# Kernel tuning notes

Measured on AMD Instinct MI355X. Metric: run time of the kernel, lower is better.

## Reference

```python
import jax, jax.numpy as jnp
import numpy as np

B, E, H, F, L, A = 256, 1024, 1024, 2048, 196, 512
C_RATIO, H_RATIO = 0.5, 0.5


def setup_inputs() -> dict:
    key = jax.random.key(0)
    ks = jax.random.split(key, 20)
    u = lambda k, shape: jax.random.uniform(k, shape, jnp.float32, -0.1, 0.1)
    return {
        "xt": jax.random.normal(ks[0], (B, E), jnp.float32),
        "att_seq": jax.random.normal(ks[1], (B, L, F), jnp.float32),
        "h": jax.random.normal(ks[2], (B, H), jnp.float32),
        "c": jax.random.normal(ks[3], (B, H), jnp.float32),
        "Wi": u(ks[4], (4 * H, E)), "bi": u(ks[5], (4 * H,)),
        "Wh": u(ks[6], (4 * H, H)), "bh": u(ks[7], (4 * H,)),
        "Wz": u(ks[8], (4 * H, F)), "bz": u(ks[9], (4 * H,)),
        "Wa": u(ks[10], (A, F)), "ba": u(ks[11], (A,)),
        "Wha": u(ks[12], (A, H)), "bha": u(ks[13], (A,)),
        "Wo": u(ks[14], (1, A)), "bo": u(ks[15], (1,)),
    }


def reference(xt, att_seq, h, c, Wi, bi, Wh, bh, Wz, bz, Wa, ba, Wha, bha, Wo, bo):
    # attention scoring: tanh(att_2_att_h(att) + h_2_att_h(h)) -> scalar per location
    att_linear = jnp.einsum("blf,af->bla", att_seq, Wa) + ba          # [B,L,A]
    h_linear = h @ Wha.T + bha                                        # [B,A]
    att_h = jnp.tanh(att_linear + h_linear[:, None, :])               # [B,L,A]
    scores = jnp.einsum("bla,a->bl", att_h, Wo[0]) + bo[0]            # [B,L]
    w = jax.nn.softmax(scores, axis=-1)                               # [B,L]
    z = jnp.einsum("bl,blf->bf", w, att_seq)                          # [B,F] context

    # fused LSTM gates
    sums = (xt @ Wi.T + bi) + (h @ Wh.T + bh) + (z @ Wz.T + bz)       # [B,4H]
    i_g = jax.nn.sigmoid(sums[:, 0 * H:1 * H])
    f_g = jax.nn.sigmoid(sums[:, 1 * H:2 * H])
    o_g = jax.nn.sigmoid(sums[:, 2 * H:3 * H])
    g = jnp.tanh(sums[:, 3 * H:4 * H])

    # zoneout blending (training mode; dropout prob is 0 -> identity)
    next_c = c * C_RATIO + (1.0 - C_RATIO) * (f_g * c + i_g * g)
    next_h = h * H_RATIO + (1.0 - H_RATIO) * (o_g * jnp.tanh(next_c))
    return next_h, next_h, next_c  # (output, state_h, state_c)
```

## Files before the change

### kernel.cpp

```cpp
#include <hip/hip_runtime.h>

#define B_ 256
#define E_ 1024
#define H_ 1024
#define F_ 2048
#define L_ 196
#define A_ 512
#define ML (B_ * L_)

typedef __attribute__((ext_vector_type(8))) short short8;
typedef __attribute__((ext_vector_type(4))) float f32x4;

__device__ __forceinline__ unsigned short f2bf(float x) {
  unsigned u = __float_as_uint(x);
  unsigned r = (u + 0x7FFFu + ((u >> 16) & 1u)) >> 16;
  return (unsigned short)r;
}
__device__ __forceinline__ float bf2f(unsigned short u) {
  return __uint_as_float((unsigned)u << 16);
}
__device__ __forceinline__ float fast_tanh(float x) {
  x = fminf(fmaxf(x, -15.f), 15.f);
  float e = __expf(2.f * x);
  return (e - 1.f) / (e + 1.f);
}
__device__ __forceinline__ float sigmoidf_(float x) {
  return 1.f / (1.f + __expf(-x));
}

#define GLOAD_LDS(gptr, lptr) \
  __builtin_amdgcn_global_load_lds( \
      (const __attribute__((address_space(1))) void*)(gptr), \
      (__attribute__((address_space(3))) void*)(lptr), 16, 0, 0)

#define SBAR() asm volatile("s_barrier" ::: "memory")

__global__ void cast_wx_k(const float* __restrict__ Wa, const float* __restrict__ Wha,
                          const float* __restrict__ Wi, const float* __restrict__ Wh,
                          const float* __restrict__ Wz, const float* __restrict__ xt,
                          const float* __restrict__ h,
                          unsigned short* __restrict__ WaB, unsigned short* __restrict__ WhaB,
                          unsigned short* __restrict__ WgB, unsigned short* __restrict__ AgB) {
  size_t i = ((size_t)blockIdx.x * 256 + threadIdx.x) * 8;
  const float* src;
  unsigned short* dst;
  if (i < 1048576) { src = Wa + i; dst = WaB + i; }
  else if (i < 1572864) { src = Wha + (i - 1048576); dst = WhaB + (i - 1048576); }
  else if (i < 18350080) {
    size_t off = i - 1572864;
    int row = (int)(off >> 12), col = (int)(off & 4095);
    if (col < 1024)       src = Wi + (size_t)row * 1024 + col;
    else if (col < 2048)  src = Wh + (size_t)row * 1024 + (col - 1024);
    else                  src = Wz + (size_t)row * 2048 + (col - 2048);
    dst = WgB + off;
  } else {
    size_t off = i - 18350080;
    int row = (int)(off >> 11), col = (int)(off & 2047);
    src = (col < 1024) ? (xt + (size_t)row * 1024 + col) : (h + (size_t)row * 1024 + (col - 1024));
    dst = AgB + (size_t)row * 4096 + col;
  }
  float4 a = *reinterpret_cast<const float4*>(src);
  float4 b = *reinterpret_cast<const float4*>(src + 4);
  short8 o;
  o[0] = (short)f2bf(a.x); o[1] = (short)f2bf(a.y); o[2] = (short)f2bf(a.z); o[3] = (short)f2bf(a.w);
  o[4] = (short)f2bf(b.x); o[5] = (short)f2bf(b.y); o[6] = (short)f2bf(b.z); o[7] = (short)f2bf(b.w);
  *reinterpret_cast<short8*>(dst) = o;
}

__global__ __launch_bounds__(256, 2)
void hlin_gemm_k(const unsigned short* __restrict__ AgB, const unsigned short* __restrict__ WhaB,
                 const float* __restrict__ bha, float* __restrict__ hlin) {
  __shared__ unsigned short As[2][64 * 64];
  __shared__ unsigned short Bs[2][128 * 64];
  const int tid = threadIdx.x;
  const int lane = tid & 63, wid = tid >> 6;
  const int wm = wid >> 1, wn = wid & 1;
  const int m0 = blockIdx.y * 64;
  const int n0 = blockIdx.x * 128;
  const int g16 = lane >> 4, l16 = lane & 15;
  const int l7 = l16 & 7;
  f32x4 acc[2][4] = {};

#define STAGE_HL(BUF, KK)                                                                      \
  {                                                                                            \
    _Pragma("unroll")                                                                          \
    for (int it = 0; it < 2; ++it) {                                                           \
      int idx = it * 256 + tid;                                                                \
      int row = idx >> 3;                                                                      \
      int kc = (idx & 7) ^ (row & 7);                                                          \
      GLOAD_LDS(AgB + (size_t)(m0 + row) * 4096 + 1024 + (KK) + kc * 8, &As[BUF][idx * 8]);    \
    }                                                                                          \
    _Pragma("unroll")                                                                          \
    for (int it = 0; it < 4; ++it) {                                                           \
      int idx = it * 256 + tid;                                                                \
      int row = idx >> 3;                                                                      \
      int kc = (idx & 7) ^ (row & 7);                                                          \
      GLOAD_LDS(WhaB + (size_t)(n0 + row) * 1024 + (KK) + kc * 8, &Bs[BUF][idx * 8]);          \
    }                                                                                          \
  }

  STAGE_HL(0, 0);
  STAGE_HL(1, 64);
  asm volatile("s_waitcnt vmcnt(6)" ::: "memory");
  SBAR();
  int cur = 0;
  for (int k0 = 0; k0 < 1024; k0 += 64) {
    #pragma unroll
    for (int ks = 0; ks < 2; ++ks) {
      const int ko = ((ks * 4 + g16) ^ l7) << 3;
      short8 af[2], bfr[4];
      #pragma unroll
      for (int mi = 0; mi < 2; ++mi)
        af[mi] = *reinterpret_cast<const short8*>(&As[cur][(wm * 32 + mi * 16 + l16) * 64 + ko]);
      #pragma unroll
      for (int ni = 0; ni < 4; ++ni)
        bfr[ni] = *reinterpret_cast<const short8*>(&Bs[cur][(wn * 64 + ni * 16 + l16) * 64 + ko]);
      #pragma unroll
      for (int mi = 0; mi < 2; ++mi)
        #pragma unroll
        for (int ni = 0; ni < 4; ++ni)
          acc[mi][ni] = __builtin_amdgcn_mfma_f32_16x16x32_bf16(af[mi], bfr[ni], acc[mi][ni], 0, 0, 0);
    }
    SBAR();
    if (k0 + 128 < 1024) {
      STAGE_HL(cur, k0 + 128);
      asm volatile("s_waitcnt vmcnt(6)" ::: "memory");
    } else {
      asm volatile("s_waitcnt vmcnt(0)" ::: "memory");
    }
    SBAR();
    cur ^= 1;
  }
#undef STAGE_HL

  #pragma unroll
  for (int ni = 0; ni < 4; ++ni) {
    int col = n0 + wn * 64 + ni * 16 + l16;
    float bv = bha[col];
    #pragma unroll
    for (int mi = 0; mi < 2; ++mi)
      #pragma unroll
      for (int j = 0; j < 4; ++j) {
        int m = m0 + wm * 32 + mi * 16 + g16 * 4 + j;
        hlin[(size_t)m * A_ + col] = acc[mi][ni][j] + bv;
      }
  }
}

template <bool WB>
__global__ __launch_bounds__(256, 2)
void score_fuse_k(const float* __restrict__ att, unsigned short* __restrict__ attB,
                  const unsigned short* __restrict__ WaB,
                  const float* __restrict__ hlin, const float* __restrict__ ba,
                  const float* __restrict__ Wo, float* __restrict__ scores8) {
  __shared__ unsigned short As[2][128 * 64];
  __shared__ unsigned short Bs[2][128 * 64];
  const int tid = threadIdx.x;
  const int lane = tid & 63, wid = tid >> 6;
  const int wm = wid >> 1, wn = wid & 1;
  const int logical = (blockIdx.x & 7) * 196 + (blockIdx.x >> 3);
  const int m0 = (logical >> 2) * 128;
  const int n0 = (logical & 3) * 128;
  const int g16 = lane >> 4, l16 = lane & 15;
  const int l7 = l16 & 7;
  f32x4 acc[4][4] = {};
  float4 a_reg[8];

#define LOADA(KK)                                                                        \
  {                                                                                      \
    _Pragma("unroll")                                                                    \
    for (int it = 0; it < 8; ++it) {                                                     \
      int idx = it * 256 + tid;                                                          \
      int row = idx >> 4, kf = idx & 15;                                                 \
      a_reg[it] = *reinterpret_cast<const float4*>(att + (size_t)(m0 + row) * F_ + (KK) + kf * 4); \
    }                                                                                    \
  }
#define GLDB(BUF, KK)                                                                    \
  {                                                                                      \
    _Pragma("unroll")                                                                    \
    for (int it = 0; it < 4; ++it) {                                                     \
      int idx = it * 256 + tid;                                                          \
      int row = idx >> 3;                                                                \
      int kc = (idx & 7) ^ (row & 7);                                                    \
      GLOAD_LDS(WaB + (size_t)(n0 + row) * F_ + (KK) + kc * 8, &Bs[BUF][idx * 8]);       \
    }                                                                                    \
  }
#define WRITEA(BUF, KK)                                                                  \
  {                                                                                      \
    _Pragma("unroll")                                                                    \
    for (int it = 0; it < 8; ++it) {                                                     \
      int idx = it * 256 + tid;                                                          \
      int row = idx >> 4, kf = idx & 15;                                                 \
      float4 v = a_reg[it];                                                              \
      ushort4 o;                                                                         \
      o.x = f2bf(v.x); o.y = f2bf(v.y); o.z = f2bf(v.z); o.w = f2bf(v.w);                \
      int el = row * 64 + (((kf >> 1) ^ (row & 7)) << 3) + ((kf & 1) << 2);              \
      *reinterpret_cast<ushort4*>(&As[BUF][el]) = o;                                     \
      if (WB && n0 == 0)                                                                 \
        *reinterpret_cast<ushort4*>(attB + (size_t)(m0 + row) * F_ + (KK) + kf * 4) = o; \
    }                                                                                    \
  }

  LOADA(0);
  GLDB(0, 0);
  asm volatile("s_waitcnt vmcnt(0)" ::: "memory");
  WRITEA(0, 0);
  LOADA(64);
  GLDB(1, 64);
  asm volatile("s_waitcnt lgkmcnt(0)" ::: "memory");
  SBAR();

  int cur = 0;
  for (int k0 = 0; k0 < F_; k0 += 64) {
    #pragma unroll
    for (int ks = 0; ks < 2; ++ks) {
      const int ko = ((ks * 4 + g16) ^ l7) << 3;
      short8 af[4], bfr[4];
      #pragma unroll
      for (int mi = 0; mi < 4; ++mi)
        af[mi] = *reinterpret_cast<const short8*>(&As[cur][(wm * 64 + mi * 16 + l16) * 64 + ko]);
      #pragma unroll
      for (int ni = 0; ni < 4; ++ni)
        bfr[ni] = *reinterpret_cast<const short8*>(&Bs[cur][(wn * 64 + ni * 16 + l16) * 64 + ko]);
      #pragma unroll
      for (int mi = 0; mi < 4; ++mi)
        #pragma unroll
        for (int ni = 0; ni < 4; ++ni)
          acc[mi][ni] = __builtin_amdgcn_mfma_f32_16x16x32_bf16(af[mi], bfr[ni], acc[mi][ni], 0, 0, 0);
    }
    SBAR();
    if (k0 + 64 < F_) {
      asm volatile("s_waitcnt vmcnt(0)" ::: "memory");
      WRITEA(cur ^ 1, k0 + 64);
      if (k0 + 128 < F_) {
        LOADA(k0 + 128);
        GLDB(cur, k0 + 128);
      }
      asm volatile("s_waitcnt lgkmcnt(0)" ::: "memory");
    }
    SBAR();
    cur ^= 1;
  }
#undef LOADA
#undef GLDB
#undef WRITEA

  float wo_v[4], ba_v[4];
  int a_v[4];
  #pragma unroll
  for (int ni = 0; ni < 4; ++ni) {
    int a = n0 + wn * 64 + ni * 16 + l16;
    a_v[ni] = a; wo_v[ni] = Wo[a]; ba_v[ni] = ba[a];
  }
  const int slot = (n0 >> 7) * 2 + wn;
  #pragma unroll
  for (int mi = 0; mi < 4; ++mi) {
    float rs[4];
    #pragma unroll
    for (int j = 0; j < 4; ++j) {
      int m = m0 + wm * 64 + mi * 16 + g16 * 4 + j;
      int b = m / L_;
      const float* hb = hlin + (size_t)b * A_;
      float s = 0.f;
      #pragma unroll
      for (int ni = 0; ni < 4; ++ni) {
        float v = acc[mi][ni][j] + ba_v[ni] + hb[a_v[ni]];
        s += fast_tanh(v) * wo_v[ni];
      }
      rs[j] = s;
    }
    #pragma unroll
    for (int off = 1; off < 16; off <<= 1) {
      #pragma unroll
      for (int j = 0; j < 4; ++j) rs[j] += __shfl_xor(rs[j], off);
    }
    if (l16 == 0) {
      #pragma unroll
      for (int j = 0; j < 4; ++j) {
        int m = m0 + wm * 64 + mi * 16 + g16 * 4 + j;
        scores8[(size_t)m * 8 + slot] = rs[j];
      }
    }
  }
}

__global__ __launch_bounds__(256)
void z_sm_k(const unsigned short* __restrict__ attB, const float* __restrict__ scores8,
            unsigned short* __restrict__ AgB) {
  __shared__ float sm[L_];
  const int b = blockIdx.y;
  const int tid = threadIdx.x;
  if (tid < L_) {
    const float* p = scores8 + ((size_t)b * L_ + tid) * 8;
    float4 p0 = *reinterpret_cast<const float4*>(p);
    float4 p1 = *reinterpret_cast<const float4*>(p + 4);
    sm[tid] = (p0.x + p0.y) + (p0.z + p0.w) + (p1.x + p1.y) + (p1.z + p1.w);
  }
  __syncthreads();
  float mx = -1e30f;
  for (int l = 0; l < L_; ++l) mx = fmaxf(mx, sm[l]);
  float s = 0.f;
  for (int l = 0; l < L_; ++l) s += __expf(sm[l] - mx);
  const float inv = 1.f / s;
  __syncthreads();
  if (tid < L_) sm[tid] = __expf(sm[tid] - mx) * inv;
  __syncthreads();
  const int f0 = blockIdx.x * 1024 + tid * 4;
  const unsigned short* base = attB + (size_t)b * L_ * F_ + f0;
  float a0 = 0.f, a1 = 0.f, a2 = 0.f, a3 = 0.f;
  #pragma unroll 4
  for (int l = 0; l < L_; ++l) {
    float wl = sm[l];
    ushort4 a = *reinterpret_cast<const ushort4*>(base + (size_t)l * F_);
    a0 += wl * bf2f(a.x); a1 += wl * bf2f(a.y); a2 += wl * bf2f(a.z); a3 += wl * bf2f(a.w);
  }
  ushort4 o;
  o.x = f2bf(a0); o.y = f2bf(a1); o.z = f2bf(a2); o.w = f2bf(a3);
  *reinterpret_cast<ushort4*>(AgB + (size_t)b * 4096 + 2048 + f0) = o;
}

__global__ __launch_bounds__(256)
void z_sm_f32_k(const float* __restrict__ att, const float* __restrict__ scores8,
                unsigned short* __restrict__ AgB) {
  __shared__ float sm[L_];
  const int b = blockIdx.y;
  const int tid = threadIdx.x;
  if (tid < L_) {
    const float* p = scores8 + ((size_t)b * L_ + tid) * 8;
    float4 p0 = *reinterpret_cast<const float4*>(p);
    float4 p1 = *reinterpret_cast<const float4*>(p + 4);
    sm[tid] = (p0.x + p0.y) + (p0.z + p0.w) + (p1.x + p1.y) + (p1.z + p1.w);
  }
  __syncthreads();
  float mx = -1e30f;
  for (int l = 0; l < L_; ++l) mx = fmaxf(mx, sm[l]);
  float s = 0.f;
  for (int l = 0; l < L_; ++l) s += __expf(sm[l] - mx);
  const float inv = 1.f / s;
  __syncthreads();
  if (tid < L_) sm[tid] = __expf(sm[tid] - mx) * inv;
  __syncthreads();
  const int f0 = blockIdx.x * 1024 + tid * 4;
  const float* base = att + (size_t)b * L_ * F_ + f0;
  float a0 = 0.f, a1 = 0.f, a2 = 0.f, a3 = 0.f;
  #pragma unroll 4
  for (int l = 0; l < L_; ++l) {
    float wl = sm[l];
    float4 a = *reinterpret_cast<const float4*>(base + (size_t)l * F_);
    a0 += wl * a.x; a1 += wl * a.y; a2 += wl * a.z; a3 += wl * a.w;
  }
  ushort4 o;
  o.x = f2bf(a0); o.y = f2bf(a1); o.z = f2bf(a2); o.w = f2bf(a3);
  *reinterpret_cast<ushort4*>(AgB + (size_t)b * 4096 + 2048 + f0) = o;
}

__global__ __launch_bounds__(256, 4)
void gates_gemm_k(const unsigned short* __restrict__ AgB, const unsigned short* __restrict__ WgB,
                  const float* __restrict__ bi, const float* __restrict__ bh,
                  const float* __restrict__ bz, float* __restrict__ sums) {
  __shared__ unsigned short As[2][64 * 64];
  __shared__ unsigned short Bs[2][64 * 64];
  const int tid = threadIdx.x;
  const int lane = tid & 63, wid = tid >> 6;
  const int wm = wid >> 1, wn = wid & 1;
  const int m0 = blockIdx.y * 64;
  const int n0 = blockIdx.x * 64;
  const int g16 = lane >> 4, l16 = lane & 15;
  const int l7 = l16 & 7;
  f32x4 acc[2][2] = {};

#define STAGE_GG(BUF, KK)                                                               \
  {                                                                                     \
    _Pragma("unroll")                                                                   \
    for (int it = 0; it < 2; ++it) {                                                    \
      int idx = it * 256 + tid;                                                         \
      int row = idx >> 3;                                                               \
      int kc = (idx & 7) ^ (row & 7);                                                   \
      GLOAD_LDS(AgB + (size_t)(m0 + row) * 4096 + (KK) + kc * 8, &As[BUF][idx * 8]);    \
      GLOAD_LDS(WgB + (size_t)(n0 + row) * 4096 + (KK) + kc * 8, &Bs[BUF][idx * 8]);    \
    }                                                                                   \
  }

  STAGE_GG(0, 0);
  STAGE_GG(1, 64);
  asm volatile("s_waitcnt vmcnt(4)" ::: "memory");
  SBAR();
  int cur = 0;
  for (int k0 = 0; k0 < 4096; k0 += 64) {
    #pragma unroll
    for (int ks = 0; ks < 2; ++ks) {
      const int ko = ((ks * 4 + g16) ^ l7) << 3;
      short8 af[2], bfr[2];
      #pragma unroll
      for (int mi = 0; mi < 2; ++mi)
        af[mi] = *reinterpret_cast<const short8*>(&As[cur][(wm * 32 + mi * 16 + l16) * 64 + ko]);
      #pragma unroll
      for (int ni = 0; ni < 2; ++ni)
        bfr[ni] = *reinterpret_cast<const short8*>(&Bs[cur][(wn * 32 + ni * 16 + l16) * 64 + ko]);
      #pragma unroll
      for (int mi = 0; mi < 2; ++mi)
        #pragma unroll
        for (int ni = 0; ni < 2; ++ni)
          acc[mi][ni] = __builtin_amdgcn_mfma_f32_16x16x32_bf16(af[mi], bfr[ni], acc[mi][ni], 0, 0, 0);
    }
    SBAR();
    if (k0 + 128 < 4096) {
      STAGE_GG(cur, k0 + 128);
      asm volatile("s_waitcnt vmcnt(4)" ::: "memory");
    } else {
      asm volatile("s_waitcnt vmcnt(0)" ::: "memory");
    }
    SBAR();
    cur ^= 1;
  }
#undef STAGE_GG

  #pragma unroll
  for (int ni = 0; ni < 2; ++ni) {
    int col = n0 + wn * 32 + ni * 16 + l16;
    float bsum = bi[col] + bh[col] + bz[col];
    #pragma unroll
    for (int mi = 0; mi < 2; ++mi)
      #pragma unroll
      for (int j = 0; j < 4; ++j) {
        int m = m0 + wm * 32 + mi * 16 + g16 * 4 + j;
        sums[(size_t)m * 4096 + col] = acc[mi][ni][j] + bsum;
      }
  }
}

__global__ void final_k(const float* __restrict__ sums, const float* __restrict__ h,
                        const float* __restrict__ c, float* __restrict__ out) {
  int i = blockIdx.x * 256 + threadIdx.x;
  int b = i >> 10, hh = i & 1023;
  const float* srow = sums + (size_t)b * 4096;
  float ig = sigmoidf_(srow[hh]);
  float fg = sigmoidf_(srow[1024 + hh]);
  float og = sigmoidf_(srow[2048 + hh]);
  float g  = fast_tanh(srow[3072 + hh]);
  float cv = c[i], hv = h[i];
  float nc = 0.5f * cv + 0.5f * (fg * cv + ig * g);
  float nh = 0.5f * hv + 0.5f * (og * fast_tanh(nc));
  out[i] = nh;
  out[B_ * H_ + i] = nh;
  out[2 * B_ * H_ + i] = nc;
}

extern "C" void kernel_launch(void* const* d_in, const int* in_sizes, int n_in,
                              void* d_out, int out_size, void* d_ws, size_t ws_size,
                              hipStream_t stream) {
  const float* xt  = (const float*)d_in[0];
  const float* att = (const float*)d_in[1];
  const float* h   = (const float*)d_in[2];
  const float* c   = (const float*)d_in[3];
  const float* Wi  = (const float*)d_in[4];
  const float* bi  = (const float*)d_in[5];
  const float* Wh  = (const float*)d_in[6];
  const float* bh  = (const float*)d_in[7];
  const float* Wz  = (const float*)d_in[8];
  const float* bz  = (const float*)d_in[9];
  const float* Wa  = (const float*)d_in[10];
  const float* ba  = (const float*)d_in[11];
  const float* Wha = (const float*)d_in[12];
  const float* bha = (const float*)d_in[13];
  const float* Wo  = (const float*)d_in[14];

  char* ws = (char*)d_ws;
  const size_t MB = (size_t)1 << 20;
  unsigned short* WaB  = (unsigned short*)(ws);
  unsigned short* WhaB = (unsigned short*)(ws + 2 * MB);
  unsigned short* WgB  = (unsigned short*)(ws + 3 * MB);
  unsigned short* AgB  = (unsigned short*)(ws + 35 * MB);
  float* hlin    = (float*)(ws + 37 * MB);
  float* scores8 = (float*)(ws + 38 * MB);
  float* sums    = (float*)(ws + 40 * MB);
  unsigned short* attB = (unsigned short*)(ws + 48 * MB);
  const bool BIG = ws_size >= 245 * MB;
  float* out = (float*)d_out;

  cast_wx_k<<<9216, 256, 0, stream>>>(Wa, Wha, Wi, Wh, Wz, xt, h, WaB, WhaB, WgB, AgB);
  hlin_gemm_k<<<dim3(4, 4), 256, 0, stream>>>(AgB, WhaB, bha, hlin);
  if (BIG) {
    score_fuse_k<true><<<(ML / 128) * (A_ / 128), 256, 0, stream>>>(att, attB, WaB, hlin, ba, Wo, scores8);
    z_sm_k<<<dim3(2, B_), 256, 0, stream>>>(attB, scores8, AgB);
  } else {
    score_fuse_k<false><<<(ML / 128) * (A_ / 128), 256, 0, stream>>>(att, attB, WaB, hlin, ba, Wo, scores8);
    z_sm_f32_k<<<dim3(2, B_), 256, 0, stream>>>(att, scores8, AgB);
  }
  gates_gemm_k<<<dim3(64, 4), 256, 0, stream>>>(AgB, WgB, bi, bh, bz, sums);
  final_k<<<B_ * H_ / 256, 256, 0, stream>>>(sums, h, c, out);
}
```

Before: 418.2 us.

## Deepen score GEMM A-prefetch to two register sets and drop bf16 att copy

The score GEMM now keeps two register sets for the fp32 attention tile and issues global loads two K-steps ahead, using partial vmcnt waits so the loads overlap MFMA work. The main loop is unrolled by two with explicit LDS buffer indices. The path that wrote a bf16 copy of att_seq and read it back in z_sm_k is removed, so z_sm_f32_k always rereads the fp32 attention tensor. This saves the bf16 write traffic but doubles the read bytes in the context reduction and raises register pressure in the GEMM.

```diff
diff --git a/kernel.cpp b/kernel.cpp
--- a/kernel.cpp
+++ b/kernel.cpp
@@ -147,10 +147,8 @@
   }
 }
 
-template <bool WB>
 __global__ __launch_bounds__(256, 2)
-void score_fuse_k(const float* __restrict__ att, unsigned short* __restrict__ attB,
-                  const unsigned short* __restrict__ WaB,
+void score_fuse_k(const float* __restrict__ att, const unsigned short* __restrict__ WaB,
                   const float* __restrict__ hlin, const float* __restrict__ ba,
                   const float* __restrict__ Wo, float* __restrict__ scores8) {
   __shared__ unsigned short As[2][128 * 64];
@@ -164,15 +162,15 @@
   const int g16 = lane >> 4, l16 = lane & 15;
   const int l7 = l16 & 7;
   f32x4 acc[4][4] = {};
-  float4 a_reg[8];
-
-#define LOADA(KK)                                                                        \
+  float4 Ra[8], Rb[8];
+
+#define LOADA(REG, KK)                                                                   \
   {                                                                                      \
     _Pragma("unroll")                                                                    \
     for (int it = 0; it < 8; ++it) {                                                     \
       int idx = it * 256 + tid;                                                          \
       int row = idx >> 4, kf = idx & 15;                                                 \
-      a_reg[it] = *reinterpret_cast<const float4*>(att + (size_t)(m0 + row) * F_ + (KK) + kf * 4); \
+      REG[it] = *reinterpret_cast<const float4*>(att + (size_t)(m0 + row) * F_ + (KK) + kf * 4); \
     }                                                                                    \
   }
 #define GLDB(BUF, KK)                                                                    \
@@ -185,65 +183,77 @@
       GLOAD_LDS(WaB + (size_t)(n0 + row) * F_ + (KK) + kc * 8, &Bs[BUF][idx * 8]);       \
     }                                                                                    \
   }
-#define WRITEA(BUF, KK)                                                                  \
+#define WRITEA(BUF, REG)                                                                 \
   {                                                                                      \
     _Pragma("unroll")                                                                    \
     for (int it = 0; it < 8; ++it) {                                                     \
       int idx = it * 256 + tid;                                                          \
       int row = idx >> 4, kf = idx & 15;                                                 \
-      float4 v = a_reg[it];                                                              \
+      float4 v = REG[it];                                                                \
       ushort4 o;                                                                         \
       o.x = f2bf(v.x); o.y = f2bf(v.y); o.z = f2bf(v.z); o.w = f2bf(v.w);                \
       int el = row * 64 + (((kf >> 1) ^ (row & 7)) << 3) + ((kf & 1) << 2);              \
       *reinterpret_cast<ushort4*>(&As[BUF][el]) = o;                                     \
-      if (WB && n0 == 0)                                                                 \
-        *reinterpret_cast<ushort4*>(attB + (size_t)(m0 + row) * F_ + (KK) + kf * 4) = o; \
     }                                                                                    \
   }
-
-  LOADA(0);
-  GLDB(0, 0);
-  asm volatile("s_waitcnt vmcnt(0)" ::: "memory");
-  WRITEA(0, 0);
-  LOADA(64);
-  GLDB(1, 64);
+#define COMPUTE(BUF)                                                                     \
+  {                                                                                      \
+    _Pragma("unroll")                                                                    \
+    for (int ks = 0; ks < 2; ++ks) {                                                     \
+      const int ko = ((ks * 4 + g16) ^ l7) << 3;                                         \
+      short8 af[4], bfr[4];                                                              \
+      _Pragma("unroll")                                                                  \
+      for (int mi = 0; mi < 4; ++mi)                                                     \
+        af[mi] = *reinterpret_cast<const short8*>(&As[BUF][(wm * 64 + mi * 16 + l16) * 64 + ko]); \
+      _Pragma("unroll")                                                                  \
+      for (int ni = 0; ni < 4; ++ni)                                                     \
+        bfr[ni] = *reinterpret_cast<const short8*>(&Bs[BUF][(wn * 64 + ni * 16 + l16) * 64 + ko]); \
+      _Pragma("unroll")                                                                  \
+      for (int mi = 0; mi < 4; ++mi)                                                     \
+        _Pragma("unroll")                                                                \
+        for (int ni = 0; ni < 4; ++ni)                                                   \
+          acc[mi][ni] = __builtin_amdgcn_mfma_f32_16x16x32_bf16(af[mi], bfr[ni], acc[mi][ni], 0, 0, 0); \
+    }                                                                                    \
+  }
+
+  LOADA(Ra, 0);  GLDB(0, 0);
+  LOADA(Rb, 64); GLDB(1, 64);
+  asm volatile("s_waitcnt vmcnt(12)" ::: "memory");
+  WRITEA(0, Ra);
   asm volatile("s_waitcnt lgkmcnt(0)" ::: "memory");
   SBAR();
 
-  int cur = 0;
-  for (int k0 = 0; k0 < F_; k0 += 64) {
-    #pragma unroll
-    for (int ks = 0; ks < 2; ++ks) {
-      const int ko = ((ks * 4 + g16) ^ l7) << 3;
-      short8 af[4], bfr[4];
-      #pragma unroll
-      for (int mi = 0; mi < 4; ++mi)
-        af[mi] = *reinterpret_cast<const short8*>(&As[cur][(wm * 64 + mi * 16 + l16) * 64 + ko]);
-      #pragma unroll
-      for (int ni = 0; ni < 4; ++ni)
-        bfr[ni] = *reinterpret_cast<const short8*>(&Bs[cur][(wn * 64 + ni * 16 + l16) * 64 + ko]);
-      #pragma unroll
-      for (int mi = 0; mi < 4; ++mi)
-        #pragma unroll
-        for (int ni = 0; ni < 4; ++ni)
-          acc[mi][ni] = __builtin_amdgcn_mfma_f32_16x16x32_bf16(af[mi], bfr[ni], acc[mi][ni], 0, 0, 0);
-    }
-    SBAR();
-    if (k0 + 64 < F_) {
+  for (int p = 0; p < 16; ++p) {
+    const int t = 2 * p;
+    COMPUTE(0);
+    SBAR();
+    if (t + 2 < 32) {
+      LOADA(Ra, (t + 2) * 64); GLDB(0, (t + 2) * 64);
+      asm volatile("s_waitcnt vmcnt(12)" ::: "memory");
+    } else {
       asm volatile("s_waitcnt vmcnt(0)" ::: "memory");
-      WRITEA(cur ^ 1, k0 + 64);
-      if (k0 + 128 < F_) {
-        LOADA(k0 + 128);
-        GLDB(cur, k0 + 128);
-      }
-      asm volatile("s_waitcnt lgkmcnt(0)" ::: "memory");
-    }
-    SBAR();
-    cur ^= 1;
+    }
+    WRITEA(1, Rb);
+    asm volatile("s_waitcnt lgkmcnt(0)" ::: "memory");
+    SBAR();
+    COMPUTE(1);
+    SBAR();
+    if (t + 3 < 32) {
+      LOADA(Rb, (t + 3) * 64); GLDB(1, (t + 3) * 64);
+      asm volatile("s_waitcnt vmcnt(12)" ::: "memory");
+    } else {
+      asm volatile("s_waitcnt vmcnt(0)" ::: "memory");
+    }
+    if (t + 2 < 32) {
+      WRITEA(0, Ra);
+    }
+    asm volatile("s_waitcnt lgkmcnt(0)" ::: "memory");
+    SBAR();
   }
 #undef LOADA
 #undef GLDB
 #undef WRITEA
+#undef COMPUTE
 
   float wo_v[4], ba_v[4];
   int a_v[4];
@@ -282,41 +292,6 @@
       }
     }
   }
-}
-
-__global__ __launch_bounds__(256)
-void z_sm_k(const unsigned short* __restrict__ attB, const float* __restrict__ scores8,
-            unsigned short* __restrict__ AgB) {
-  __shared__ float sm[L_];
-  const int b = blockIdx.y;
-  const int tid = threadIdx.x;
-  if (tid < L_) {
-    const float* p = scores8 + ((size_t)b * L_ + tid) * 8;
-    float4 p0 = *reinterpret_cast<const float4*>(p);
-    float4 p1 = *reinterpret_cast<const float4*>(p + 4);
-    sm[tid] = (p0.x + p0.y) + (p0.z + p0.w) + (p1.x + p1.y) + (p1.z + p1.w);
-  }
-  __syncthreads();
-  float mx = -1e30f;
-  for (int l = 0; l < L_; ++l) mx = fmaxf(mx, sm[l]);
-  float s = 0.f;
-  for (int l = 0; l < L_; ++l) s += __expf(sm[l] - mx);
-  const float inv = 1.f / s;
-  __syncthreads();
-  if (tid < L_) sm[tid] = __expf(sm[tid] - mx) * inv;
-  __syncthreads();
-  const int f0 = blockIdx.x * 1024 + tid * 4;
-  const unsigned short* base = attB + (size_t)b * L_ * F_ + f0;
-  float a0 = 0.f, a1 = 0.f, a2 = 0.f, a3 = 0.f;
-  #pragma unroll 4
-  for (int l = 0; l < L_; ++l) {
-    float wl = sm[l];
-    ushort4 a = *reinterpret_cast<const ushort4*>(base + (size_t)l * F_);
-    a0 += wl * bf2f(a.x); a1 += wl * bf2f(a.y); a2 += wl * bf2f(a.z); a3 += wl * bf2f(a.w);
-  }
-  ushort4 o;
-  o.x = f2bf(a0); o.y = f2bf(a1); o.z = f2bf(a2); o.w = f2bf(a3);
-  *reinterpret_cast<ushort4*>(AgB + (size_t)b * 4096 + 2048 + f0) = o;
 }
 
 __global__ __launch_bounds__(256)
@@ -474,19 +449,12 @@
   float* hlin    = (float*)(ws + 37 * MB);
   float* scores8 = (float*)(ws + 38 * MB);
   float* sums    = (float*)(ws + 40 * MB);
-  unsigned short* attB = (unsigned short*)(ws + 48 * MB);
-  const bool BIG = ws_size >= 245 * MB;
   float* out = (float*)d_out;
 
   cast_wx_k<<<9216, 256, 0, stream>>>(Wa, Wha, Wi, Wh, Wz, xt, h, WaB, WhaB, WgB, AgB);
   hlin_gemm_k<<<dim3(4, 4), 256, 0, stream>>>(AgB, WhaB, bha, hlin);
-  if (BIG) {
-    score_fuse_k<true><<<(ML / 128) * (A_ / 128), 256, 0, stream>>>(att, attB, WaB, hlin, ba, Wo, scores8);
-    z_sm_k<<<dim3(2, B_), 256, 0, stream>>>(attB, scores8, AgB);
-  } else {
-    score_fuse_k<false><<<(ML / 128) * (A_ / 128), 256, 0, stream>>>(att, attB, WaB, hlin, ba, Wo, scores8);
-    z_sm_f32_k<<<dim3(2, B_), 256, 0, stream>>>(att, scores8, AgB);
-  }
+  score_fuse_k<<<(ML / 128) * (A_ / 128), 256, 0, stream>>>(att, WaB, hlin, ba, Wo, scores8);
+  z_sm_f32_k<<<dim3(2, B_), 256, 0, stream>>>(att, scores8, AgB);
   gates_gemm_k<<<dim3(64, 4), 256, 0, stream>>>(AgB, WgB, bi, bh, bz, sums);
   final_k<<<B_ * H_ / 256, 256, 0, stream>>>(sums, h, c, out);
 }
```

Result: faster. 380.1 us (-9.1%).
